# Optimization experiments

Hardware: AMD Instinct MI355X
Metric: run time of the kernel (lower is better)

The kernel has to match this reference:

```python
import jax, jax.numpy as jnp
import numpy as np

EPS = 1e-06


def setup_inputs() -> dict:
    key = jax.random.key(0)
    k1, k2 = jax.random.split(key)
    x = jax.random.normal(k1, (256, 4096), dtype=jnp.float32)
    # learned parameter, init matches torch.randn(...) * 0.1
    shapelets = jax.random.normal(k2, (8, 16, 128), dtype=jnp.float32) * 0.1
    return {"x": x, "shapelets": shapelets}


def reference(x, shapelets):
    B, T = x.shape
    C, Kc, L = shapelets.shape
    nwin = T - L + 1  # stride-1 unfold

    # sliding windows: [B, nwin, L] (same materialization as torch unfold)
    idx = jnp.arange(nwin)[:, None] + jnp.arange(L)[None, :]
    x_win = x[:, idx]

    # z-normalize each window (population std, unbiased=False)
    mu_x = jnp.mean(x_win, axis=2, keepdims=True)
    var_x = jnp.mean((x_win - mu_x) ** 2, axis=2, keepdims=True)
    std_x = jnp.sqrt(var_x) + EPS
    x_norm = (x_win - mu_x) / std_x

    # z-normalize shapelets per class/shapelet
    mu_s = jnp.mean(shapelets, axis=2, keepdims=True)
    var_s = jnp.mean((shapelets - mu_s) ** 2, axis=2, keepdims=True)
    std_s = jnp.sqrt(var_s) + EPS
    s_norm = (shapelets - mu_s) / std_s

    # normalized cross-correlation: [B, nwin, C, Kc]
    corr = jnp.einsum('btl,ckl->btck', x_norm, s_norm) / L

    # max over window positions, concat classes -> [B, C*Kc]
    max_vals = jnp.max(corr, axis=1)  # [B, C, Kc]
    return max_vals.reshape(B, C * Kc)
```

## Files before the change

### kernel.cpp

```cpp
#include <hip/hip_runtime.h>
#include <hip/hip_bf16.h>

typedef __attribute__((ext_vector_type(8))) short short8;
typedef __attribute__((ext_vector_type(4))) float float4v;

#define T_LEN 4096
#define L_LEN 128
#define NWIN  3969
#define CK    128
#define W_BLK 128
#define NCHUNK 32

#define CSUM_OFF  32768

__device__ __forceinline__ unsigned short f2bf(float f) {
    unsigned u = __float_as_uint(f);
    u += 0x7fffu + ((u >> 16) & 1u);
    return (unsigned short)(u >> 16);
}
__device__ __forceinline__ float bf2f(unsigned short b) {
    return __uint_as_float(((unsigned)b) << 16);
}

__global__ void prep_init(const float* __restrict__ sh,
                          unsigned short* __restrict__ wsB,
                          float* __restrict__ csum,
                          unsigned* __restrict__ oenc) {
    const int t = threadIdx.x;
    if (blockIdx.x < 128) {
        oenc[blockIdx.x * 256 + t]       = 0u;
        oenc[blockIdx.x * 256 + 128 + t] = 0u;
        return;
    }
    const int ck = blockIdx.x - 128;
    const int l  = t;
    __shared__ float rs[2], rq[2], rc[2];
    const int lane = t & 63, wv = t >> 6;

    float v = sh[ck * L_LEN + l];
    float s = v, q = v * v;
    #pragma unroll
    for (int off = 32; off >= 1; off >>= 1) {
        s += __shfl_xor(s, off);
        q += __shfl_xor(q, off);
    }
    if (lane == 0) { rs[wv] = s; rq[wv] = q; }
    __syncthreads();
    float sm = rs[0] + rs[1], sq = rq[0] + rq[1];
    float mu  = sm * (1.f / L_LEN);
    float var = fmaxf(sq * (1.f / L_LEN) - mu * mu, 0.f);
    float inv = 1.f / (sqrtf(var) + 1e-6f);

    unsigned short b = f2bf((v - mu) * inv);
    const int nt = ck >> 4, n = ck & 15;
    const int kt = l >> 5, qd = (l >> 3) & 3, jj = l & 7;
    wsB[((((nt * 4 + kt) * 64) + qd * 16 + n) << 3) + jj] = b;

    float cv = bf2f(b);
    #pragma unroll
    for (int off = 32; off >= 1; off >>= 1) cv += __shfl_xor(cv, off);
    if (lane == 0) rc[wv] = cv;
    __syncthreads();
    if (t == 0) csum[ck] = rc[0] + rc[1];
}

__global__ __launch_bounds__(256, 4)
void conv_main(const float* __restrict__ x,
               const unsigned short* __restrict__ wsB,
               const float* __restrict__ csum,
               unsigned* __restrict__ oenc) {
    __shared__ alignas(16) unsigned short xb[8][256];
    __shared__ float PS[257], PQ[257];
    __shared__ float wts[4], wtq[4];
    __shared__ float2 st[W_BLK];
    __shared__ float wmax[4][64];

    const int tid   = threadIdx.x;
    const int row   = blockIdx.x >> 5;
    const int chunk = blockIdx.x & 31;
    const int T0    = (chunk < 31) ? chunk * W_BLK : (NWIN - W_BLK);

    float v = 0.f;
    if (tid < 255) {
        v = x[row * T_LEN + T0 + tid];
        unsigned short b = f2bf(v);
        #pragma unroll
        for (int c = 0; c < 8; ++c) {
            int i = tid - c;
            if (i >= 0) xb[c][i] = b;
        }
    }

    const int lane = tid & 63;
    const int wv   = tid >> 6;
    float s = v, q = v * v;
    #pragma unroll
    for (int off = 1; off < 64; off <<= 1) {
        float ts = __shfl_up(s, off);
        float tq = __shfl_up(q, off);
        if (lane >= off) { s += ts; q += tq; }
    }
    if (lane == 63) { wts[wv] = s; wtq[wv] = q; }
    __syncthreads();
    float os = 0.f, oq = 0.f;
    #pragma unroll
    for (int w = 0; w < 3; ++w) if (w < wv) { os += wts[w]; oq += wtq[w]; }
    PS[tid + 1] = os + s;
    PQ[tid + 1] = oq + q;
    if (tid == 0) { PS[0] = 0.f; PQ[0] = 0.f; }
    __syncthreads();

    if (tid < W_BLK) {
        float S  = PS[tid + L_LEN] - PS[tid];
        float Q  = PQ[tid + L_LEN] - PQ[tid];
        float mu = S * (1.f / L_LEN);
        float var = fmaxf(Q * (1.f / L_LEN) - mu * mu, 0.f);
        float sd  = sqrtf(var) + 1e-6f;
        st[tid] = make_float2(mu, 1.f / (sd * (float)L_LEN));
    }

    const int nhalf  = wv & 1;
    const int mgroup = wv >> 1;
    const int abase  = (lane & 15) + (lane >> 4);

    float cck[4];
    #pragma unroll
    for (int nt4 = 0; nt4 < 4; ++nt4)
        cck[nt4] = csum[(nhalf * 4 + nt4) * 16 + (lane & 15)];

    float4v acc[4][4];
    #pragma unroll
    for (int a = 0; a < 4; ++a)
        #pragma unroll
        for (int b = 0; b < 4; ++b)
            acc[a][b] = float4v{0.f, 0.f, 0.f, 0.f};

    const short8* Bp = (const short8*)wsB;
    #pragma unroll
    for (int kt = 0; kt < 4; ++kt) {
        short8 bq[4];
        #pragma unroll
        for (int nt4 = 0; nt4 < 4; ++nt4)
            bq[nt4] = Bp[((nhalf * 4 + nt4) * 4 + kt) * 64 + lane];
        #pragma unroll
        for (int mi = 0; mi < 4; ++mi) {
            int j = mgroup * 4 + mi;
            short8 af = *(const short8*)&xb[j][8 * (abase + 4 * kt)];
            #pragma unroll
            for (int nt4 = 0; nt4 < 4; ++nt4)
                acc[mi][nt4] = __builtin_amdgcn_mfma_f32_16x16x32_bf16(
                    af, bq[nt4], acc[mi][nt4], 0, 0, 0);
        }
    }
    __syncthreads();

    float vmax[4] = {-1e30f, -1e30f, -1e30f, -1e30f};
    const int q4 = (lane >> 4) * 4;
    #pragma unroll
    for (int mi = 0; mi < 4; ++mi) {
        int j = mgroup * 4 + mi;
        #pragma unroll
        for (int r = 0; r < 4; ++r) {
            float2 s2 = st[j + 8 * (q4 + r)];
            #pragma unroll
            for (int nt4 = 0; nt4 < 4; ++nt4) {
                float corr = (acc[mi][nt4][r] - s2.x * cck[nt4]) * s2.y;
                vmax[nt4] = fmaxf(vmax[nt4], corr);
            }
        }
    }
    #pragma unroll
    for (int nt4 = 0; nt4 < 4; ++nt4) {
        float vx = vmax[nt4];
        vx = fmaxf(vx, __shfl_xor(vx, 16));
        vx = fmaxf(vx, __shfl_xor(vx, 32));
        if (lane < 16) wmax[wv][nt4 * 16 + lane] = vx;
    }
    __syncthreads();
    if (tid < 128) {
        int ck = tid;
        int nh = ck >> 6, idx = ck & 63;
        float vx = fmaxf(wmax[nh][idx], wmax[nh + 2][idx]);
        vx = fmaxf(vx, 0.f);
        atomicMax(&oenc[row * CK + ck], __float_as_uint(vx));
    }
}

extern "C" void kernel_launch(void* const* d_in, const int* in_sizes, int n_in,
                              void* d_out, int out_size, void* d_ws, size_t ws_size,
                              hipStream_t stream) {
    (void)in_sizes; (void)n_in; (void)out_size; (void)ws_size;
    const float* x  = (const float*)d_in[0];
    const float* sh = (const float*)d_in[1];
    unsigned short* wsB = (unsigned short*)d_ws;
    float* csum = (float*)((char*)d_ws + CSUM_OFF);
    unsigned* oenc = (unsigned*)d_out;

    prep_init<<<256, 128, 0, stream>>>(sh, wsB, csum, oenc);
    conv_main<<<256 * NCHUNK, 256, 0, stream>>>(x, wsB, csum, oenc);
}
```

Before: 95.32 us.

## Process one full row per block with register-resident shapelet fragments

Replaces the 8192-block chunked convolution with 256 blocks that each handle a whole row. All bf16 shapelet fragments stay in registers and the 32 window chunks are looped over inside the block. Window stats come from a single row-wide prefix sum followed by a sliding update. The mean-correction term is dropped because the normalized shapelets sum to zero, and the atomicMax output plus its zero-init pass are replaced by a direct store. The trade-off is only 256 blocks, which may underfill the GPU, along with heavy register use (128 VGPRs for B fragments) and a large LDS footprint per block.

```diff
diff --git a/kernel.cpp b/kernel.cpp
--- a/kernel.cpp
+++ b/kernel.cpp
@@ -8,34 +8,19 @@
 #define L_LEN 128
 #define NWIN  3969
 #define CK    128
-#define W_BLK 128
-#define NCHUNK 32
-
-#define CSUM_OFF  32768
 
 __device__ __forceinline__ unsigned short f2bf(float f) {
     unsigned u = __float_as_uint(f);
     u += 0x7fffu + ((u >> 16) & 1u);
     return (unsigned short)(u >> 16);
 }
-__device__ __forceinline__ float bf2f(unsigned short b) {
-    return __uint_as_float(((unsigned)b) << 16);
-}
 
-__global__ void prep_init(const float* __restrict__ sh,
-                          unsigned short* __restrict__ wsB,
-                          float* __restrict__ csum,
-                          unsigned* __restrict__ oenc) {
-    const int t = threadIdx.x;
-    if (blockIdx.x < 128) {
-        oenc[blockIdx.x * 256 + t]       = 0u;
-        oenc[blockIdx.x * 256 + 128 + t] = 0u;
-        return;
-    }
-    const int ck = blockIdx.x - 128;
-    const int l  = t;
-    __shared__ float rs[2], rq[2], rc[2];
-    const int lane = t & 63, wv = t >> 6;
+__global__ void prep_sh(const float* __restrict__ sh,
+                        unsigned short* __restrict__ wsB) {
+    const int ck = blockIdx.x;
+    const int l  = threadIdx.x;
+    __shared__ float rs[2], rq[2];
+    const int lane = l & 63, wv = l >> 6;
 
     float v = sh[ck * L_LEN + l];
     float s = v, q = v * v;
@@ -50,139 +35,149 @@
     float mu  = sm * (1.f / L_LEN);
     float var = fmaxf(sq * (1.f / L_LEN) - mu * mu, 0.f);
     float inv = 1.f / (sqrtf(var) + 1e-6f);
-
     unsigned short b = f2bf((v - mu) * inv);
     const int nt = ck >> 4, n = ck & 15;
     const int kt = l >> 5, qd = (l >> 3) & 3, jj = l & 7;
     wsB[((((nt * 4 + kt) * 64) + qd * 16 + n) << 3) + jj] = b;
-
-    float cv = bf2f(b);
-    #pragma unroll
-    for (int off = 32; off >= 1; off >>= 1) cv += __shfl_xor(cv, off);
-    if (lane == 0) rc[wv] = cv;
-    __syncthreads();
-    if (t == 0) csum[ck] = rc[0] + rc[1];
 }
 
-__global__ __launch_bounds__(256, 4)
-void conv_main(const float* __restrict__ x,
-               const unsigned short* __restrict__ wsB,
-               const float* __restrict__ csum,
-               unsigned* __restrict__ oenc) {
-    __shared__ alignas(16) unsigned short xb[8][256];
-    __shared__ float PS[257], PQ[257];
-    __shared__ float wts[4], wtq[4];
-    __shared__ float2 st[W_BLK];
-    __shared__ float wmax[4][64];
+__global__ __launch_bounds__(512, 2)
+void conv_row(const float* __restrict__ x,
+              const unsigned short* __restrict__ wsB,
+              float* __restrict__ out) {
+    __shared__ alignas(16) unsigned short xb[8][T_LEN];
+    __shared__ float sty[T_LEN];
+    __shared__ float PSs[513], PQs[513];
+    __shared__ float grpS[8], grpQ[8];
+    __shared__ float wmax[8][CK];
 
-    const int tid   = threadIdx.x;
-    const int row   = blockIdx.x >> 5;
-    const int chunk = blockIdx.x & 31;
-    const int T0    = (chunk < 31) ? chunk * W_BLK : (NWIN - W_BLK);
+    const int tid  = threadIdx.x;
+    const int lane = tid & 63;
+    const int wv   = tid >> 6;
+    const int row  = blockIdx.x;
+    const float4* xr4 = (const float4*)(x + row * T_LEN);
 
-    float v = 0.f;
-    if (tid < 255) {
-        v = x[row * T_LEN + T0 + tid];
-        unsigned short b = f2bf(v);
+    short8 Bf[8][4];
+    {
+        const short8* Bp = (const short8*)wsB;
         #pragma unroll
-        for (int c = 0; c < 8; ++c) {
-            int i = tid - c;
-            if (i >= 0) xb[c][i] = b;
-        }
+        for (int nt = 0; nt < 8; ++nt)
+            #pragma unroll
+            for (int kt = 0; kt < 4; ++kt)
+                Bf[nt][kt] = Bp[(nt * 4 + kt) * 64 + lane];
     }
 
-    const int lane = tid & 63;
-    const int wv   = tid >> 6;
-    float s = v, q = v * v;
+    float v[16];
+    {
+        float4 a0 = xr4[2 * tid];
+        float4 a1 = xr4[2 * tid + 1];
+        float4 a2 = make_float4(0.f, 0.f, 0.f, 0.f), a3 = a2;
+        if (tid < 511) { a2 = xr4[2 * tid + 2]; a3 = xr4[2 * tid + 3]; }
+        v[0]=a0.x; v[1]=a0.y; v[2]=a0.z;  v[3]=a0.w;
+        v[4]=a1.x; v[5]=a1.y; v[6]=a1.z;  v[7]=a1.w;
+        v[8]=a2.x; v[9]=a2.y; v[10]=a2.z; v[11]=a2.w;
+        v[12]=a3.x; v[13]=a3.y; v[14]=a3.z; v[15]=a3.w;
+    }
+    unsigned short bb[16];
+    #pragma unroll
+    for (int i = 0; i < 16; ++i) bb[i] = f2bf(v[i]);
+    #pragma unroll
+    for (int c = 0; c < 8; ++c) {
+        short8 w8;
+        #pragma unroll
+        for (int j = 0; j < 8; ++j) w8[j] = (short)bb[c + j];
+        *(short8*)&xb[c][8 * tid] = w8;
+    }
+
+    float s = 0.f, q = 0.f;
+    #pragma unroll
+    for (int i = 0; i < 8; ++i) { s += v[i]; q += v[i] * v[i]; }
+    float is = s, iq = q;
     #pragma unroll
     for (int off = 1; off < 64; off <<= 1) {
-        float ts = __shfl_up(s, off);
-        float tq = __shfl_up(q, off);
-        if (lane >= off) { s += ts; q += tq; }
+        float ts = __shfl_up(is, off);
+        float tq = __shfl_up(iq, off);
+        if (lane >= off) { is += ts; iq += tq; }
     }
-    if (lane == 63) { wts[wv] = s; wtq[wv] = q; }
+    if (lane == 63) { grpS[wv] = is; grpQ[wv] = iq; }
     __syncthreads();
     float os = 0.f, oq = 0.f;
     #pragma unroll
-    for (int w = 0; w < 3; ++w) if (w < wv) { os += wts[w]; oq += wtq[w]; }
-    PS[tid + 1] = os + s;
-    PQ[tid + 1] = oq + q;
-    if (tid == 0) { PS[0] = 0.f; PQ[0] = 0.f; }
+    for (int w = 0; w < 7; ++w) if (w < wv) { os += grpS[w]; oq += grpQ[w]; }
+    PSs[tid] = os + is - s;
+    PQs[tid] = oq + iq - q;
+    if (tid == 511) { PSs[512] = os + is; PQs[512] = oq + iq; }
     __syncthreads();
 
-    if (tid < W_BLK) {
-        float S  = PS[tid + L_LEN] - PS[tid];
-        float Q  = PQ[tid + L_LEN] - PQ[tid];
-        float mu = S * (1.f / L_LEN);
-        float var = fmaxf(Q * (1.f / L_LEN) - mu * mu, 0.f);
-        float sd  = sqrtf(var) + 1e-6f;
-        st[tid] = make_float2(mu, 1.f / (sd * (float)L_LEN));
-    }
-
-    const int nhalf  = wv & 1;
-    const int mgroup = wv >> 1;
-    const int abase  = (lane & 15) + (lane >> 4);
-
-    float cck[4];
-    #pragma unroll
-    for (int nt4 = 0; nt4 < 4; ++nt4)
-        cck[nt4] = csum[(nhalf * 4 + nt4) * 16 + (lane & 15)];
-
-    float4v acc[4][4];
-    #pragma unroll
-    for (int a = 0; a < 4; ++a)
+    if (tid < 497) {
+        float S = PSs[tid + 16] - PSs[tid];
+        float Q = PQs[tid + 16] - PQs[tid];
+        float4 b0 = make_float4(0.f, 0.f, 0.f, 0.f), b1 = b0;
+        if (tid <= 495) { b0 = xr4[2 * tid + 32]; b1 = xr4[2 * tid + 33]; }
+        float xn[8] = {b0.x, b0.y, b0.z, b0.w, b1.x, b1.y, b1.z, b1.w};
         #pragma unroll
-        for (int b = 0; b < 4; ++b)
-            acc[a][b] = float4v{0.f, 0.f, 0.f, 0.f};
-
-    const short8* Bp = (const short8*)wsB;
-    #pragma unroll
-    for (int kt = 0; kt < 4; ++kt) {
-        short8 bq[4];
-        #pragma unroll
-        for (int nt4 = 0; nt4 < 4; ++nt4)
-            bq[nt4] = Bp[((nhalf * 4 + nt4) * 4 + kt) * 64 + lane];
-        #pragma unroll
-        for (int mi = 0; mi < 4; ++mi) {
-            int j = mgroup * 4 + mi;
-            short8 af = *(const short8*)&xb[j][8 * (abase + 4 * kt)];
-            #pragma unroll
-            for (int nt4 = 0; nt4 < 4; ++nt4)
-                acc[mi][nt4] = __builtin_amdgcn_mfma_f32_16x16x32_bf16(
-                    af, bq[nt4], acc[mi][nt4], 0, 0, 0);
+        for (int e = 0; e < 8; ++e) {
+            int w = 8 * tid + e;
+            if (w < NWIN) {
+                float mu  = S * (1.f / L_LEN);
+                float var = fmaxf(Q * (1.f / L_LEN) - mu * mu, 0.f);
+                float sd  = sqrtf(var) + 1e-6f;
+                sty[w] = 1.f / (sd * (float)L_LEN);
+                S += xn[e] - v[e];
+                Q += xn[e] * xn[e] - v[e] * v[e];
+            }
         }
     }
     __syncthreads();
 
-    float vmax[4] = {-1e30f, -1e30f, -1e30f, -1e30f};
-    const int q4 = (lane >> 4) * 4;
+    const int abase = (lane & 15) + (lane >> 4);
+    const int q4    = (lane >> 4) * 4;
+    float vmax[8];
     #pragma unroll
-    for (int mi = 0; mi < 4; ++mi) {
-        int j = mgroup * 4 + mi;
+    for (int nt = 0; nt < 8; ++nt) vmax[nt] = -1e30f;
+
+    #pragma unroll 1
+    for (int ci = 0; ci < 32; ++ci) {
+        const int T0 = (ci < 31) ? ci * 128 : (NWIN - 128);
+        const int e0 = T0 + wv;
+        const int c  = e0 & 7;
+        const int b8 = e0 >> 3;
+
+        float4v acc[8];
+        #pragma unroll
+        for (int nt = 0; nt < 8; ++nt) acc[nt] = float4v{0.f, 0.f, 0.f, 0.f};
+
+        #pragma unroll
+        for (int kt = 0; kt < 4; ++kt) {
+            const short8 af = *(const short8*)&xb[c][8 * (b8 + abase + 4 * kt)];
+            #pragma unroll
+            for (int nt = 0; nt < 8; ++nt)
+                acc[nt] = __builtin_amdgcn_mfma_f32_16x16x32_bf16(
+                    af, Bf[nt][kt], acc[nt], 0, 0, 0);
+        }
+
         #pragma unroll
         for (int r = 0; r < 4; ++r) {
-            float2 s2 = st[j + 8 * (q4 + r)];
+            const float sr = sty[e0 + 8 * (q4 + r)];
             #pragma unroll
-            for (int nt4 = 0; nt4 < 4; ++nt4) {
-                float corr = (acc[mi][nt4][r] - s2.x * cck[nt4]) * s2.y;
-                vmax[nt4] = fmaxf(vmax[nt4], corr);
-            }
+            for (int nt = 0; nt < 8; ++nt)
+                vmax[nt] = fmaxf(vmax[nt], acc[nt][r] * sr);
         }
     }
+
     #pragma unroll
-    for (int nt4 = 0; nt4 < 4; ++nt4) {
-        float vx = vmax[nt4];
+    for (int nt = 0; nt < 8; ++nt) {
+        float vx = vmax[nt];
         vx = fmaxf(vx, __shfl_xor(vx, 16));
         vx = fmaxf(vx, __shfl_xor(vx, 32));
-        if (lane < 16) wmax[wv][nt4 * 16 + lane] = vx;
+        if (lane < 16) wmax[wv][nt * 16 + lane] = vx;
     }
     __syncthreads();
-    if (tid < 128) {
-        int ck = tid;
-        int nh = ck >> 6, idx = ck & 63;
-        float vx = fmaxf(wmax[nh][idx], wmax[nh + 2][idx]);
-        vx = fmaxf(vx, 0.f);
-        atomicMax(&oenc[row * CK + ck], __float_as_uint(vx));
+    if (tid < CK) {
+        float m = wmax[0][tid];
+        #pragma unroll
+        for (int w = 1; w < 8; ++w) m = fmaxf(m, wmax[w][tid]);
+        out[row * CK + tid] = m;
     }
 }
 
@@ -193,9 +188,8 @@
     const float* x  = (const float*)d_in[0];
     const float* sh = (const float*)d_in[1];
     unsigned short* wsB = (unsigned short*)d_ws;
-    float* csum = (float*)((char*)d_ws + CSUM_OFF);
-    unsigned* oenc = (unsigned*)d_out;
+    float* out = (float*)d_out;
 
-    prep_init<<<256, 128, 0, stream>>>(sh, wsB, csum, oenc);
-    conv_main<<<256 * NCHUNK, 256, 0, stream>>>(x, wsB, csum, oenc);
+    prep_sh<<<128, 128, 0, stream>>>(sh, wsB);
+    conv_row<<<256, 512, 0, stream>>>(x, wsB, out);
 }
```

New measurement: 83.02 us. 1.15x faster.
